# Kernel optimization log

Hardware: AMD Instinct MI355X
Metric: run time of the kernel (lower is better)

Reference implementation:

```python
import jax, jax.numpy as jnp
import numpy as np

N_NODES = 100000
N_EDGES = 1600000
HEADS = 8
CH = 16
NEG_SLOPE = 0.2


def setup_inputs() -> dict:
    key = jax.random.key(0)
    ks = jax.random.split(key, 8)
    x = jax.random.normal(ks[0], (N_NODES, 16), dtype=jnp.float32)
    edge_index = jax.random.randint(ks[1], (2, N_EDGES), 0, N_NODES, dtype=jnp.int64)
    W = jax.random.normal(ks[2], (16, HEADS * CH), dtype=jnp.float32) * 0.25
    att_src = jax.random.normal(ks[3], (HEADS, CH), dtype=jnp.float32) * 0.25
    att_dst = jax.random.normal(ks[4], (HEADS, CH), dtype=jnp.float32) * 0.25
    bias = jax.random.normal(ks[5], (HEADS * CH,), dtype=jnp.float32) * 0.1
    fc_w = jax.random.normal(ks[6], (HEADS * CH, 5), dtype=jnp.float32) * 0.1
    fc_b = jax.random.normal(ks[7], (5,), dtype=jnp.float32) * 0.1
    return {"x": x, "edge_index": edge_index, "W": W, "att_src": att_src,
            "att_dst": att_dst, "bias": bias, "fc_w": fc_w, "fc_b": fc_b}


def reference(x, edge_index, W, att_src, att_dst, bias, fc_w, fc_b):
    N = x.shape[0]
    # PyG GATConv default: add self loops
    loops = jnp.arange(N, dtype=edge_index.dtype)
    src = jnp.concatenate([edge_index[0], loops])
    dst = jnp.concatenate([edge_index[1], loops])

    h = (x @ W).reshape(N, HEADS, CH)                 # [N,H,C]
    a_src = jnp.einsum('nhc,hc->nh', h, att_src)      # [N,H]
    a_dst = jnp.einsum('nhc,hc->nh', h, att_dst)      # [N,H]

    e = a_src[src] + a_dst[dst]                       # [E,H]
    e = jax.nn.leaky_relu(e, NEG_SLOPE)
    # segment softmax over edges grouped by destination node
    e_max = jax.ops.segment_max(e, dst, num_segments=N)
    e_exp = jnp.exp(e - e_max[dst])
    denom = jax.ops.segment_sum(e_exp, dst, num_segments=N)
    alpha = e_exp / (denom[dst] + 1e-16)              # [E,H]

    msg = alpha[:, :, None] * h[src]                  # [E,H,C]
    out = jax.ops.segment_sum(msg, dst, num_segments=N)  # [N,H,C]
    out = out.reshape(N, HEADS * CH) + bias           # concat heads + bias

    out = jax.nn.relu(out)
    # dropout is identity in eval mode
    logits = out @ fc_w + fc_b                        # [N,5]
    return jax.nn.log_softmax(logits, axis=1)
```

## Files before the change

kernel.cpp:

```cpp
#include <hip/hip_runtime.h>
#include <hip/hip_bf16.h>
#include <hip/hip_fp16.h>
#include <math.h>

#define N_NODES 100000
#define N_EDGES 1600000
#define HEADS 8
#define HC 128
#define LOG2E 1.44269504f

#define DPB 64
#define NB 1563
#define NBP (NB + 1)
#define NCH 512
#define EPC (N_EDGES / NCH)
#define CAPS 1664
#define WSTR (CAPS + 4)
#define NA 196

__global__ __launch_bounds__(512) void k_prep(
    const float* __restrict__ x, const float* __restrict__ W,
    const float* __restrict__ att_s, const float* __restrict__ att_d,
    const int* __restrict__ ei,
    unsigned short* __restrict__ a_srcb, float* __restrict__ a_dst,
    uint4* __restrict__ x2b,
    int* __restrict__ offs, unsigned* __restrict__ stg) {
    __shared__ int smem[2048 + EPC];
    __shared__ int ws8[8];
    int t = threadIdx.x;
    if (blockIdx.x >= NCH) {
        float* sM = (float*)smem;
        if (t < 256) {
            int k = t >> 4, h2 = t & 15;
            const float* av = (h2 < 8) ? att_s : att_d;
            int h = h2 & 7;
            float s = 0.f;
#pragma unroll
            for (int c = 0; c < 16; ++c)
                s = fmaf(W[k * HC + h * 16 + c], av[h * 16 + c], s);
            sM[k * 16 + h2] = s * LOG2E;
        }
        __syncthreads();
        int node = (blockIdx.x - NCH) * 512 + t;
        if (node < N_NODES) {
            const float4* xr = (const float4*)(x + node * 16);
            float4 x0 = xr[0], x1 = xr[1], x2 = xr[2], x3 = xr[3];
            float xv[16] = {x0.x, x0.y, x0.z, x0.w, x1.x, x1.y, x1.z, x1.w,
                            x2.x, x2.y, x2.z, x2.w, x3.x, x3.y, x3.z, x3.w};
            union { uint4 u[2]; __hip_bfloat162 b[8]; } px;
#pragma unroll
            for (int k = 0; k < 8; ++k)
                px.b[k] = __float22bfloat162_rn(float2{xv[2 * k], xv[2 * k + 1]});
            x2b[node * 2] = px.u[0];
            x2b[node * 2 + 1] = px.u[1];
            float oo[16];
#pragma unroll
            for (int h2 = 0; h2 < 16; ++h2) {
                float o = 0.f;
#pragma unroll
                for (int k = 0; k < 16; ++k) o = fmaf(xv[k], sM[k * 16 + h2], o);
                oo[h2] = o;
            }
            union { uint4 u; unsigned short s[8]; } pb;
#pragma unroll
            for (int h = 0; h < 8; ++h)
                pb.s[h] = __bfloat16_as_ushort(__float2bfloat16(oo[h]));
            *(uint4*)(a_srcb + (size_t)node * 8) = pb.u;
            float4 d0 = {oo[8], oo[9], oo[10], oo[11]};
            float4 d1 = {oo[12], oo[13], oo[14], oo[15]};
            *(float4*)(a_dst + (size_t)node * 8) = d0;
            *(float4*)(a_dst + (size_t)node * 8 + 4) = d1;
        }
    } else {
        int* hist = smem;
        unsigned* entries = (unsigned*)(smem + 2048);
        int c = blockIdx.x;
        hist[t] = 0; hist[t + 512] = 0; hist[t + 1024] = 0; hist[t + 1536] = 0;
        __syncthreads();
        int beg = c * EPC, end = beg + EPC;
        for (int e = beg + t; e < end; e += 512)
            atomicAdd(&hist[ei[N_EDGES + e] >> 6], 1);
        __syncthreads();
        int i0 = 4 * t;
        int v0 = hist[i0], v1 = hist[i0 + 1], v2 = hist[i0 + 2], v3 = hist[i0 + 3];
        int s1 = v0 + v1, s2 = s1 + v2, T = s2 + v3;
        int lane = t & 63, wv = t >> 6;
        int inc = T;
#pragma unroll
        for (int off = 1; off < 64; off <<= 1) {
            int y = __shfl_up(inc, off);
            if (lane >= off) inc += y;
        }
        if (lane == 63) ws8[wv] = inc;
        __syncthreads();
        int wbase = 0;
        for (int k = 0; k < wv; ++k) wbase += ws8[k];
        int e0 = wbase + inc - T;
        hist[i0] = e0; hist[i0 + 1] = e0 + v0;
        hist[i0 + 2] = e0 + s1; hist[i0 + 3] = e0 + s2;
        __syncthreads();
        int row = c * NBP;
        for (int b = t; b < NB; b += 512) offs[row + b] = hist[b];
        if (t == 0) offs[row + NB] = EPC;
        __syncthreads();
        for (int e = beg + t; e < end; e += 512) {
            int src = ei[e], dst = ei[N_EDGES + e];
            int pos = atomicAdd(&hist[dst >> 6], 1);
            entries[pos] = ((unsigned)(dst & 63) << 17) | (unsigned)src;
        }
        __syncthreads();
        unsigned* so = stg + beg;
        for (int i = t; i < EPC; i += 512) so[i] = entries[i];
    }
}

__global__ __launch_bounds__(512) void k_gather(
    const __hip_bfloat162* __restrict__ x2b,
    const unsigned short* __restrict__ a_srcb, const float* __restrict__ W,
    const float* __restrict__ a_dst,
    const int* __restrict__ offs, const unsigned* __restrict__ stg,
    const float* __restrict__ bias, const float* __restrict__ fc_w,
    const float* __restrict__ fc_b, float* __restrict__ out) {
    __shared__ __align__(16) unsigned short wst[8 * WSTR];
    __shared__ __align__(16) unsigned estg[CAPS];
    __shared__ __align__(16) int sbuf[CAPS];
    __shared__ __align__(16) float sW[16 * HC];
    __shared__ __align__(16) float sad[8 * DPB];
    __shared__ int hist[DPB];
    __shared__ int bs[DPB + 1];
    __shared__ int ws8[8];
    int* cstage = sbuf;
    int* o0_s = sbuf;
    int* myb_s = sbuf + 512;
    int b = blockIdx.x, t = threadIdx.x;
    int d0 = b * DPB;
    for (int i = t; i < 16 * HC; i += 512) {
        int c = i & 127, k = i >> 7;
        int blk = c >> 3;
        int sb = blk ^ ((blk >> 2) & 3);
        sW[k * HC + sb * 8 + (c & 7)] = W[i];
    }
    sad[t] = (d0 * 8 + t < N_NODES * 8) ? a_dst[(size_t)d0 * 8 + t] : 0.f;
    int lane = t & 63, wv = t >> 6;
    {
        int o0 = offs[t * NBP + b];
        int len = offs[t * NBP + b + 1] - o0;
        o0_s[t] = o0;
        int inc = len;
#pragma unroll
        for (int off = 1; off < 64; off <<= 1) {
            int y = __shfl_up(inc, off);
            if (lane >= off) inc += y;
        }
        if (lane == 63) ws8[wv] = inc;
        __syncthreads();
        int wbase = 0;
        for (int k = 0; k < wv; ++k) wbase += ws8[k];
        myb_s[t] = wbase + inc - len;
        if (t == 511) myb_s[NCH] = wbase + inc;
    }
    if (t < DPB) hist[t] = (d0 + t < N_NODES) ? 1 : 0;
    __syncthreads();
    int tot = myb_s[NCH];
    for (int i = t; i < tot; i += 512) {
        int lo = 0, hi = NCH - 1;
#pragma unroll
        for (int s = 0; s < 9; ++s) {
            int mid = (lo + hi + 1) >> 1;
            if (myb_s[mid] <= i) lo = mid; else hi = mid - 1;
        }
        unsigned u = stg[lo * EPC + o0_s[lo] + (i - myb_s[lo])];
        estg[i] = u;
        atomicAdd(&hist[u >> 17], 1);
    }
    __syncthreads();
    if (t < 64) {
        int gd = d0 + t;
        bool val = gd < N_NODES;
        int len = hist[t];
        int plen = (len + 3) & ~3;
        int iv = plen;
#pragma unroll
        for (int off = 1; off < 64; off <<= 1) {
            int y = __shfl_up(iv, off);
            if (t >= off) iv += y;
        }
        int excl = iv - plen;
        bs[t] = excl;
        if (t == 63) bs[64] = iv;
        hist[t] = excl + (val ? 1 : 0);
        for (int k = len; k < plen; ++k) {
            cstage[excl + k] = 0;
#pragma unroll
            for (int h = 0; h < 8; ++h) wst[h * WSTR + excl + k] = 0;
        }
        if (val) {
            cstage[excl] = gd;
            union { uint4 v; __hip_bfloat162 b2[4]; } pa;
            pa.v = *(const uint4*)(a_srcb + (size_t)gd * 8);
            const float* adp = sad + t * 8;
            float4 ad0 = *(const float4*)(adp);
            float4 ad1 = *(const float4*)(adp + 4);
            float2 s01 = __bfloat1622float2(pa.b2[0]);
            float2 s23 = __bfloat1622float2(pa.b2[1]);
            float2 s45 = __bfloat1622float2(pa.b2[2]);
            float2 s67 = __bfloat1622float2(pa.b2[3]);
            float e[8] = {s01.x + ad0.x, s01.y + ad0.y, s23.x + ad0.z,
                          s23.y + ad0.w, s45.x + ad1.x, s45.y + ad1.y,
                          s67.x + ad1.z, s67.y + ad1.w};
#pragma unroll
            for (int h = 0; h < 8; ++h) {
                float eh = fmaxf(e[h], 0.2f * e[h]);
                wst[h * WSTR + excl] =
                    __half_as_ushort(__float2half(exp2f(eh)));
            }
        }
    }
    __syncthreads();
    for (int i = t; i < tot; i += 512) {
        unsigned u = estg[i];
        int pos = atomicAdd(&hist[u >> 17], 1);
        int s = (int)(u & 0x1FFFF);
        int dl = (int)(u >> 17);
        cstage[pos] = s;
        union { uint4 v; __hip_bfloat162 b2[4]; } pa;
        pa.v = *(const uint4*)(a_srcb + (size_t)s * 8);
        const float* adp = sad + dl * 8;
        float4 ad0 = *(const float4*)(adp);
        float4 ad1 = *(const float4*)(adp + 4);
        float2 s01 = __bfloat1622float2(pa.b2[0]);
        float2 s23 = __bfloat1622float2(pa.b2[1]);
        float2 s45 = __bfloat1622float2(pa.b2[2]);
        float2 s67 = __bfloat1622float2(pa.b2[3]);
        float e[8] = {s01.x + ad0.x, s01.y + ad0.y, s23.x + ad0.z, s23.y + ad0.w,
                      s45.x + ad1.x, s45.y + ad1.y, s67.x + ad1.z, s67.y + ad1.w};
#pragma unroll
        for (int h = 0; h < 8; ++h) {
            float eh = fmaxf(e[h], 0.2f * e[h]);
            wst[h * WSTR + pos] = __half_as_ushort(__float2half(exp2f(eh)));
        }
    }
    __syncthreads();
    int q = t & 15, g = t >> 4;
    int head = q >> 1, i8 = q & 1;
    int c0 = head * 16 + i8 * 8;
    int blk0 = c0 >> 3;
    int sw0 = (blk0 ^ ((blk0 >> 2) & 3)) * 8;
    const unsigned short* wrow = wst + head * WSTR;
    int xofs = i8 * 16;
    const char* xb = (const char*)x2b;
    float bb[8], fwv[8][5], fbv[5];
#pragma unroll
    for (int m = 0; m < 8; ++m) bb[m] = bias[c0 + m];
#pragma unroll
    for (int m = 0; m < 8; ++m)
#pragma unroll
        for (int jj = 0; jj < 5; ++jj) fwv[m][jj] = fc_w[(c0 + m) * 5 + jj];
#pragma unroll
    for (int jj = 0; jj < 5; ++jj) fbv[jj] = fc_b[jj];
    for (int l4 = 0; l4 < 2; ++l4) {
        int l = g * 2 + l4;
        int gd = d0 + l;
        if (gd >= N_NODES) break;
        int beg = bs[l], end = bs[l + 1];
        float A[8] = {0.f, 0.f, 0.f, 0.f, 0.f, 0.f, 0.f, 0.f};
        float wsum = 0.f;
        auto acc = [&](const uint4& xv, float w) {
            union { uint4 v; __hip_bfloat162 b2[4]; } xx; xx.v = xv;
            float2 f0 = __bfloat1622float2(xx.b2[0]);
            float2 f1 = __bfloat1622float2(xx.b2[1]);
            float2 f2 = __bfloat1622float2(xx.b2[2]);
            float2 f3 = __bfloat1622float2(xx.b2[3]);
            A[0] = fmaf(w, f0.x, A[0]); A[1] = fmaf(w, f0.y, A[1]);
            A[2] = fmaf(w, f1.x, A[2]); A[3] = fmaf(w, f1.y, A[3]);
            A[4] = fmaf(w, f2.x, A[4]); A[5] = fmaf(w, f2.y, A[5]);
            A[6] = fmaf(w, f3.x, A[6]); A[7] = fmaf(w, f3.y, A[7]);
        };
        for (int j = beg; j < end; j += 4) {
            int4 cs = *(const int4*)(cstage + j);
            uint2 wu = *(const uint2*)(wrow + j);
            union { uint2 u2; __half2 h2[2]; } wq; wq.u2 = wu;
            float2 w01 = __half22float2(wq.h2[0]);
            float2 w23 = __half22float2(wq.h2[1]);
            uint4 xv0 = *(const uint4*)(xb + ((cs.x << 5) + xofs));
            uint4 xv1 = *(const uint4*)(xb + ((cs.y << 5) + xofs));
            uint4 xv2 = *(const uint4*)(xb + ((cs.z << 5) + xofs));
            uint4 xv3 = *(const uint4*)(xb + ((cs.w << 5) + xofs));
            acc(xv0, w01.x); acc(xv1, w01.y);
            acc(xv2, w23.x); acc(xv3, w23.y);
            wsum += (w01.x + w01.y) + (w23.x + w23.y);
        }
        float inv = 1.f / (wsum + 1e-16f);
#pragma unroll
        for (int m = 0; m < 8; ++m) A[m] *= inv;
        float ov[8] = {0.f, 0.f, 0.f, 0.f, 0.f, 0.f, 0.f, 0.f};
#pragma unroll
        for (int m = 0; m < 8; ++m) {
            float a = A[m];
            float ap = __shfl_xor(A[m], 1);
            const float* w0r = sW + (i8 * 8 + m) * HC + sw0;
            const float* w1r = sW + ((1 - i8) * 8 + m) * HC + sw0;
#pragma unroll
            for (int o = 0; o < 8; ++o) ov[o] = fmaf(a, w0r[o], ov[o]);
#pragma unroll
            for (int o = 0; o < 8; ++o) ov[o] = fmaf(ap, w1r[o], ov[o]);
        }
#pragma unroll
        for (int m = 0; m < 8; ++m) ov[m] = fmaxf(ov[m] + bb[m], 0.f);
        float p[5];
#pragma unroll
        for (int jj = 0; jj < 5; ++jj) {
            float sacc = 0.f;
#pragma unroll
            for (int m = 0; m < 8; ++m) sacc = fmaf(ov[m], fwv[m][jj], sacc);
            p[jj] = sacc;
        }
#pragma unroll
        for (int off = 8; off >= 1; off >>= 1)
#pragma unroll
            for (int jj = 0; jj < 5; ++jj) p[jj] += __shfl_xor(p[jj], off);
        if (q == 0) {
            float lg[5], mx = -1e30f;
#pragma unroll
            for (int jj = 0; jj < 5; ++jj) {
                lg[jj] = p[jj] + fbv[jj];
                mx = fmaxf(mx, lg[jj]);
            }
            float sum = 0.f;
#pragma unroll
            for (int jj = 0; jj < 5; ++jj) sum += __expf(lg[jj] - mx);
            float ls = mx + __logf(sum);
#pragma unroll
            for (int jj = 0; jj < 5; ++jj) out[gd * 5 + jj] = lg[jj] - ls;
        }
    }
}

extern "C" void kernel_launch(void* const* d_in, const int* in_sizes, int n_in,
                              void* d_out, int out_size, void* d_ws, size_t ws_size,
                              hipStream_t stream) {
    const float* x     = (const float*)d_in[0];
    const int*   ei    = (const int*)d_in[1];
    const float* W     = (const float*)d_in[2];
    const float* att_s = (const float*)d_in[3];
    const float* att_d = (const float*)d_in[4];
    const float* bias  = (const float*)d_in[5];
    const float* fc_w  = (const float*)d_in[6];
    const float* fc_b  = (const float*)d_in[7];
    float* out = (float*)d_out;

    char* ws = (char*)d_ws;
    size_t off = 0;
    auto carve = [&](size_t bytes) {
        void* p = ws + off;
        off = (off + bytes + 255) & ~(size_t)255;
        return p;
    };
    unsigned short* a_srcb = (unsigned short*)carve((size_t)N_NODES * HEADS * 2);
    float*    a_dst = (float*)   carve((size_t)N_NODES * HEADS * 4);
    uint4*    x2b   = (uint4*)   carve((size_t)N_NODES * 32);
    int*      offs  = (int*)     carve((size_t)NCH * NBP * 4);
    unsigned* stg   = (unsigned*)carve((size_t)N_EDGES * 4);

    k_prep<<<NCH + NA, 512, 0, stream>>>(x, W, att_s, att_d, ei,
                                         a_srcb, a_dst, x2b, offs, stg);
    k_gather<<<NB, 512, 0, stream>>>((const __hip_bfloat162*)x2b, a_srcb, W,
                                     a_dst, offs, stg, bias, fc_w, fc_b, out);
}
```

Baseline: 163.2 us.

## Stage gathered source features into LDS per half-block before aggregation

```diff
diff --git a/kernel.cpp b/kernel.cpp
--- a/kernel.cpp
+++ b/kernel.cpp
@@ -16,6 +16,7 @@
 #define EPC (N_EDGES / NCH)
 #define CAPS 1664
 #define WSTR (CAPS + 4)
+#define CAPH 832
 #define NA 196
 
 __global__ __launch_bounds__(512) void k_prep(
@@ -121,14 +122,15 @@
     const int* __restrict__ offs, const unsigned* __restrict__ stg,
     const float* __restrict__ bias, const float* __restrict__ fc_w,
     const float* __restrict__ fc_b, float* __restrict__ out) {
+    __shared__ __align__(16) uint4 xst[CAPH * 2];
     __shared__ __align__(16) unsigned short wst[8 * WSTR];
-    __shared__ __align__(16) unsigned estg[CAPS];
     __shared__ __align__(16) int sbuf[CAPS];
     __shared__ __align__(16) float sW[16 * HC];
     __shared__ __align__(16) float sad[8 * DPB];
     __shared__ int hist[DPB];
     __shared__ int bs[DPB + 1];
     __shared__ int ws8[8];
+    unsigned* estg = (unsigned*)xst;
     int* cstage = sbuf;
     int* o0_s = sbuf;
     int* myb_s = sbuf + 512;
@@ -247,8 +249,7 @@
     int blk0 = c0 >> 3;
     int sw0 = (blk0 ^ ((blk0 >> 2) & 3)) * 8;
     const unsigned short* wrow = wst + head * WSTR;
-    int xofs = i8 * 16;
-    const char* xb = (const char*)x2b;
+    const uint4* x4 = (const uint4*)x2b;
     float bb[8], fwv[8][5], fbv[5];
 #pragma unroll
     for (int m = 0; m < 8; ++m) bb[m] = bias[c0 + m];
@@ -258,81 +259,91 @@
         for (int jj = 0; jj < 5; ++jj) fwv[m][jj] = fc_w[(c0 + m) * 5 + jj];
 #pragma unroll
     for (int jj = 0; jj < 5; ++jj) fbv[jj] = fc_b[jj];
-    for (int l4 = 0; l4 < 2; ++l4) {
-        int l = g * 2 + l4;
+    for (int h = 0; h < 2; ++h) {
+        int hs = bs[h * 32], he = bs[h * 32 + 32];
+        for (int i = hs + t; i < he; i += 512) {
+            int s = cstage[i];
+            int kk = (i - hs) * 2;
+            xst[kk] = x4[2 * s];
+            xst[kk + 1] = x4[2 * s + 1];
+        }
+        __syncthreads();
+        int l = h * 32 + g;
         int gd = d0 + l;
-        if (gd >= N_NODES) break;
-        int beg = bs[l], end = bs[l + 1];
-        float A[8] = {0.f, 0.f, 0.f, 0.f, 0.f, 0.f, 0.f, 0.f};
-        float wsum = 0.f;
-        auto acc = [&](const uint4& xv, float w) {
-            union { uint4 v; __hip_bfloat162 b2[4]; } xx; xx.v = xv;
-            float2 f0 = __bfloat1622float2(xx.b2[0]);
-            float2 f1 = __bfloat1622float2(xx.b2[1]);
-            float2 f2 = __bfloat1622float2(xx.b2[2]);
-            float2 f3 = __bfloat1622float2(xx.b2[3]);
-            A[0] = fmaf(w, f0.x, A[0]); A[1] = fmaf(w, f0.y, A[1]);
-            A[2] = fmaf(w, f1.x, A[2]); A[3] = fmaf(w, f1.y, A[3]);
-            A[4] = fmaf(w, f2.x, A[4]); A[5] = fmaf(w, f2.y, A[5]);
-            A[6] = fmaf(w, f3.x, A[6]); A[7] = fmaf(w, f3.y, A[7]);
-        };
-        for (int j = beg; j < end; j += 4) {
-            int4 cs = *(const int4*)(cstage + j);
-            uint2 wu = *(const uint2*)(wrow + j);
-            union { uint2 u2; __half2 h2[2]; } wq; wq.u2 = wu;
-            float2 w01 = __half22float2(wq.h2[0]);
-            float2 w23 = __half22float2(wq.h2[1]);
-            uint4 xv0 = *(const uint4*)(xb + ((cs.x << 5) + xofs));
-            uint4 xv1 = *(const uint4*)(xb + ((cs.y << 5) + xofs));
-            uint4 xv2 = *(const uint4*)(xb + ((cs.z << 5) + xofs));
-            uint4 xv3 = *(const uint4*)(xb + ((cs.w << 5) + xofs));
-            acc(xv0, w01.x); acc(xv1, w01.y);
-            acc(xv2, w23.x); acc(xv3, w23.y);
-            wsum += (w01.x + w01.y) + (w23.x + w23.y);
-        }
-        float inv = 1.f / (wsum + 1e-16f);
-#pragma unroll
-        for (int m = 0; m < 8; ++m) A[m] *= inv;
-        float ov[8] = {0.f, 0.f, 0.f, 0.f, 0.f, 0.f, 0.f, 0.f};
-#pragma unroll
-        for (int m = 0; m < 8; ++m) {
-            float a = A[m];
-            float ap = __shfl_xor(A[m], 1);
-            const float* w0r = sW + (i8 * 8 + m) * HC + sw0;
-            const float* w1r = sW + ((1 - i8) * 8 + m) * HC + sw0;
-#pragma unroll
-            for (int o = 0; o < 8; ++o) ov[o] = fmaf(a, w0r[o], ov[o]);
-#pragma unroll
-            for (int o = 0; o < 8; ++o) ov[o] = fmaf(ap, w1r[o], ov[o]);
-        }
-#pragma unroll
-        for (int m = 0; m < 8; ++m) ov[m] = fmaxf(ov[m] + bb[m], 0.f);
-        float p[5];
-#pragma unroll
-        for (int jj = 0; jj < 5; ++jj) {
-            float sacc = 0.f;
-#pragma unroll
-            for (int m = 0; m < 8; ++m) sacc = fmaf(ov[m], fwv[m][jj], sacc);
-            p[jj] = sacc;
-        }
-#pragma unroll
-        for (int off = 8; off >= 1; off >>= 1)
-#pragma unroll
-            for (int jj = 0; jj < 5; ++jj) p[jj] += __shfl_xor(p[jj], off);
-        if (q == 0) {
-            float lg[5], mx = -1e30f;
+        if (gd < N_NODES) {
+            int beg = bs[l], end = bs[l + 1];
+            float A[8] = {0.f, 0.f, 0.f, 0.f, 0.f, 0.f, 0.f, 0.f};
+            float wsum = 0.f;
+            auto acc = [&](const uint4& xv, float w) {
+                union { uint4 v; __hip_bfloat162 b2[4]; } xx; xx.v = xv;
+                float2 f0 = __bfloat1622float2(xx.b2[0]);
+                float2 f1 = __bfloat1622float2(xx.b2[1]);
+                float2 f2 = __bfloat1622float2(xx.b2[2]);
+                float2 f3 = __bfloat1622float2(xx.b2[3]);
+                A[0] = fmaf(w, f0.x, A[0]); A[1] = fmaf(w, f0.y, A[1]);
+                A[2] = fmaf(w, f1.x, A[2]); A[3] = fmaf(w, f1.y, A[3]);
+                A[4] = fmaf(w, f2.x, A[4]); A[5] = fmaf(w, f2.y, A[5]);
+                A[6] = fmaf(w, f3.x, A[6]); A[7] = fmaf(w, f3.y, A[7]);
+            };
+            for (int j = beg; j < end; j += 4) {
+                uint2 wu = *(const uint2*)(wrow + j);
+                union { uint2 u2; __half2 h2[2]; } wq; wq.u2 = wu;
+                float2 w01 = __half22float2(wq.h2[0]);
+                float2 w23 = __half22float2(wq.h2[1]);
+                int k0 = (j - hs) * 2 + i8;
+                uint4 xv0 = xst[k0];
+                uint4 xv1 = xst[k0 + 2];
+                uint4 xv2 = xst[k0 + 4];
+                uint4 xv3 = xst[k0 + 6];
+                acc(xv0, w01.x); acc(xv1, w01.y);
+                acc(xv2, w23.x); acc(xv3, w23.y);
+                wsum += (w01.x + w01.y) + (w23.x + w23.y);
+            }
+            float inv = 1.f / (wsum + 1e-16f);
+#pragma unroll
+            for (int m = 0; m < 8; ++m) A[m] *= inv;
+            float ov[8] = {0.f, 0.f, 0.f, 0.f, 0.f, 0.f, 0.f, 0.f};
+#pragma unroll
+            for (int m = 0; m < 8; ++m) {
+                float a = A[m];
+                float ap = __shfl_xor(A[m], 1);
+                const float* w0r = sW + (i8 * 8 + m) * HC + sw0;
+                const float* w1r = sW + ((1 - i8) * 8 + m) * HC + sw0;
+#pragma unroll
+                for (int o = 0; o < 8; ++o) ov[o] = fmaf(a, w0r[o], ov[o]);
+#pragma unroll
+                for (int o = 0; o < 8; ++o) ov[o] = fmaf(ap, w1r[o], ov[o]);
+            }
+#pragma unroll
+            for (int m = 0; m < 8; ++m) ov[m] = fmaxf(ov[m] + bb[m], 0.f);
+            float p[5];
 #pragma unroll
             for (int jj = 0; jj < 5; ++jj) {
-                lg[jj] = p[jj] + fbv[jj];
-                mx = fmaxf(mx, lg[jj]);
-            }
-            float sum = 0.f;
-#pragma unroll
-            for (int jj = 0; jj < 5; ++jj) sum += __expf(lg[jj] - mx);
-            float ls = mx + __logf(sum);
-#pragma unroll
-            for (int jj = 0; jj < 5; ++jj) out[gd * 5 + jj] = lg[jj] - ls;
-        }
+                float sacc = 0.f;
+#pragma unroll
+                for (int m = 0; m < 8; ++m) sacc = fmaf(ov[m], fwv[m][jj], sacc);
+                p[jj] = sacc;
+            }
+#pragma unroll
+            for (int off = 8; off >= 1; off >>= 1)
+#pragma unroll
+                for (int jj = 0; jj < 5; ++jj) p[jj] += __shfl_xor(p[jj], off);
+            if (q == 0) {
+                float lg[5], mx = -1e30f;
+#pragma unroll
+                for (int jj = 0; jj < 5; ++jj) {
+                    lg[jj] = p[jj] + fbv[jj];
+                    mx = fmaxf(mx, lg[jj]);
+                }
+                float sum = 0.f;
+#pragma unroll
+                for (int jj = 0; jj < 5; ++jj) sum += __expf(lg[jj] - mx);
+                float ls = mx + __logf(sum);
+#pragma unroll
+                for (int jj = 0; jj < 5; ++jj) out[gd * 5 + jj] = lg[jj] - ls;
+            }
+        }
+        __syncthreads();
     }
 }
 
```

After: 164.4 us. Within noise of the previous version (+0.7%).
